# Kernel tuning notes

Hardware: AMD Instinct MI355X
Metric: run time of the kernel (lower is better)

The kernel has to match this reference:

```python
import jax, jax.numpy as jnp
import numpy as np

N_PTS, N_NODES, N_CMP = 2048, 8192, 1024
CHUNK = 4  # cmp columns per scan step; bounds the [P, CHUNK, N] intermediate


def setup_inputs() -> dict:
    key = jax.random.key(0)
    k1, k2 = jax.random.split(key)
    x = jax.random.normal(k1, (N_PTS, N_NODES), dtype=jnp.float32)
    # learned edge states; EDG_NULL == 0, so mask = (states != 0)
    learned_edge_states = jax.random.randint(k2, (N_NODES, N_CMP), 0, 2, dtype=jnp.int32)
    return {"x": x, "learned_edge_states": learned_edge_states}


def _masked_colmax(x, mask):
    """x: [P, N] float; mask: [N, C] bool -> [P, C] max of x over masked nodes per column.

    Columns with no nonzero entries yield 0.0 (original leaves the zero-initialized output).
    Chunked over C to avoid materializing the full [P, N, C] tensor.
    """
    neg_inf = jnp.float32(-jnp.inf)
    P = x.shape[0]
    C = mask.shape[1]
    mask_chunks = mask.T.reshape(C // CHUNK, CHUNK, -1)  # [S, CHUNK, N]

    def step(carry, m):
        # m: [CHUNK, N]; masked max over node axis -> [P, CHUNK]
        vals = jnp.max(jnp.where(m[None, :, :], x[:, None, :], neg_inf), axis=2)
        return carry, vals

    _, out = jax.lax.scan(step, None, mask_chunks)  # [S, P, CHUNK]
    out = jnp.transpose(out, (1, 0, 2)).reshape(P, C)
    has_any = jnp.any(mask, axis=0)  # [C]
    return jnp.where(has_any[None, :], out, jnp.float32(0.0))


def reference(x, learned_edge_states):
    mask = learned_edge_states != 0
    return _masked_colmax(x, mask)
```

## Files before the change

kernel.cpp:

```cpp
#include <hip/hip_runtime.h>
#include <hip/hip_bf16.h>
#include <math.h>

#define N_PTS   2048
#define N_NODES 8192
#define N_CMP   1024
#define CAP     128
#define K_MIN   32
#define K_MAX   112

#define OFF_BITS 0
#define OFF_TOPV (1u << 20)
#define OFF_TOPI (2u << 20)
#define OFF_LEN  (3u << 20)

__device__ __forceinline__ unsigned int float_to_key(float f) {
    unsigned int b = __float_as_uint(f);
    return (b & 0x80000000u) ? ~b : (b | 0x80000000u);
}
__device__ __forceinline__ float key_to_float(unsigned int k) {
    unsigned int b = (k & 0x80000000u) ? (k ^ 0x80000000u) : ~k;
    return __uint_as_float(b);
}

__global__ __launch_bounds__(256) void pack_kernel(const int* __restrict__ states,
                                                   unsigned int* __restrict__ bitsT) {
    int t    = threadIdx.x;
    int lane = t & 63;
    int W    = blockIdx.x * 4 + (t >> 6);
    int n    = W >> 4;
    int cg   = W & 15;
    int s    = states[(size_t)n * N_CMP + cg * 64 + lane];
    unsigned long long m = __ballot(s != 0);
    if (lane == 0) {
        bitsT[n * 32 + cg * 2]     = (unsigned int)(m & 0xffffffffull);
        bitsT[n * 32 + cg * 2 + 1] = (unsigned int)(m >> 32);
    }
}

__global__ __launch_bounds__(256) void select_kernel(const float* __restrict__ x,
                                                     float* __restrict__ topval,
                                                     int* __restrict__ topidx,
                                                     int* __restrict__ toplen) {
    int p = blockIdx.x;
    int t = threadIdx.x;
    const float4* row4 = reinterpret_cast<const float4*>(x + (size_t)p * N_NODES);

    unsigned int key[32];
#pragma unroll
    for (int j = 0; j < 8; j++) {
        float4 v = row4[j * 256 + t];
        key[j * 4 + 0] = float_to_key(v.x);
        key[j * 4 + 1] = float_to_key(v.y);
        key[j * 4 + 2] = float_to_key(v.z);
        key[j * 4 + 3] = float_to_key(v.w);
    }

    __shared__ unsigned int s_cnt[2][4];
    __shared__ unsigned int s_red[4];
    __shared__ unsigned int s_key[CAP];
    __shared__ int          s_id[CAP];
    __shared__ int          s_num;

    unsigned int m = 0;
#pragma unroll
    for (int i = 0; i < 32; i++) m = max(m, key[i]);
#pragma unroll
    for (int d = 1; d < 64; d <<= 1)
        m = max(m, (unsigned int)__shfl_xor((int)m, d));
    if ((t & 63) == 0) s_red[t >> 6] = m;
    __syncthreads();
    unsigned int M = max(max(s_red[0], s_red[1]), max(s_red[2], s_red[3]));
    __syncthreads();

    unsigned int lo = 0, hi = M;
    for (int it = 0; it < 34; ++it) {
        if (hi - lo <= 1) break;
        unsigned int mid;
        if (it == 0) {
            mid = 0xC0200000u;
            if (mid >= hi) mid = hi - 1;
            if (mid <= lo) mid = lo + 1;
        } else {
            mid = lo + ((hi - lo) >> 1);
        }
        int myc = 0;
#pragma unroll
        for (int i = 0; i < 32; i++)
            myc += (int)__popcll(__ballot(key[i] >= mid));
        int par = it & 1;
        if ((t & 63) == 0) s_cnt[par][t >> 6] = (unsigned int)myc;
        __syncthreads();
        int c = (int)(s_cnt[par][0] + s_cnt[par][1] + s_cnt[par][2] + s_cnt[par][3]);
        if (c >= K_MIN) {
            lo = mid;
            if (c <= K_MAX) break;
        } else {
            hi = mid;
        }
    }
    unsigned int T = lo;

    if (t == 0) s_num = 0;
    __syncthreads();
#pragma unroll
    for (int i = 0; i < 32; i++) {
        if (key[i] >= T) {
            int pos = atomicAdd(&s_num, 1);
            if (pos < CAP) {
                s_key[pos] = key[i];
                s_id[pos]  = (i >> 2) * 1024 + (t << 2) + (i & 3);
            }
        }
    }
    __syncthreads();
    int L   = s_num;
    int len = (L > CAP) ? -1 : L;

    if (len > 0 && t < L) {
        unsigned int mk = s_key[t];
        int          mi = s_id[t];
        int r = 0;
        for (int j = 0; j < L; ++j) {
            unsigned int kj = s_key[j];
            r += (int)((kj > mk) | ((kj == mk) & (j < t)));
        }
        topval[(size_t)p * CAP + r] = key_to_float(mk);
        topidx[(size_t)p * CAP + r] = mi;
    }
    if (t == 0) toplen[p] = len;
}

__global__ __launch_bounds__(256) void probe_kernel(const float* __restrict__ x,
                                                    const unsigned int* __restrict__ bitsT,
                                                    const float* __restrict__ topval,
                                                    const int* __restrict__ topidx,
                                                    const int* __restrict__ toplen,
                                                    float* __restrict__ out) {
    int t    = threadIdx.x;
    int lane = t & 63;
    int wid  = t >> 6;
    int b    = blockIdx.x;
    int p    = b >> 2;
    int q    = b & 3;
    int cg   = q * 4 + wid;
    int c    = cg * 64 + lane;
    int w5   = c >> 5;
    int bit  = c & 31;

    __shared__ float s_v[CAP];
    __shared__ int   s_n[CAP];
    __shared__ int   s_len;

    if (t == 0) s_len = toplen[p];
    if (t < CAP) {
        s_v[t] = topval[(size_t)p * CAP + t];
        s_n[t] = topidx[(size_t)p * CAP + t];
    }
    __syncthreads();
    int len = s_len;

    float res  = 0.0f;
    bool  done = false;

    if (len >= 0) {
#pragma unroll 1
        for (int k0 = 0; k0 < len; k0 += 8) {
            int kmax = len - k0;
            if (kmax > 8) kmax = 8;
            unsigned int wb[8];
#pragma unroll
            for (int j = 0; j < 8; j++)
                if (j < kmax) wb[j] = bitsT[s_n[k0 + j] * 32 + w5];
#pragma unroll
            for (int j = 0; j < 8; j++) {
                if (j < kmax) {
                    bool hit = (wb[j] >> bit) & 1u;
                    if (!done && hit) { res = s_v[k0 + j]; done = true; }
                }
            }
            if (__all((int)done)) break;
        }
    }

    if (!done) {
        const float* row = x + (size_t)p * N_NODES;
        float mm = -INFINITY;
        for (int n = 0; n < N_NODES; n++) {
            unsigned int w = bitsT[n * 32 + w5];
            if ((w >> bit) & 1u) mm = fmaxf(mm, row[n]);
        }
        res = (mm == -INFINITY) ? 0.0f : mm;
    }

    out[(size_t)p * N_CMP + c] = res;
}

extern "C" void kernel_launch(void* const* d_in, const int* in_sizes, int n_in,
                              void* d_out, int out_size, void* d_ws, size_t ws_size,
                              hipStream_t stream) {
    const float* x      = (const float*)d_in[0];
    const int*   states = (const int*)d_in[1];
    float*       out    = (float*)d_out;

    unsigned int* bitsT  = (unsigned int*)((char*)d_ws + OFF_BITS);
    float*        topval = (float*)((char*)d_ws + OFF_TOPV);
    int*          topidx = (int*)((char*)d_ws + OFF_TOPI);
    int*          toplen = (int*)((char*)d_ws + OFF_LEN);

    pack_kernel<<<(N_NODES * (N_CMP / 64)) / 4, 256, 0, stream>>>(states, bitsT);
    select_kernel<<<N_PTS, 256, 0, stream>>>(x, topval, topidx, toplen);
    probe_kernel<<<N_PTS * 4, 256, 0, stream>>>(x, bitsT, topval, topidx, toplen, out);
}
```

Before: 146.1 us.

## Fuse pack and select kernels, vectorize pack, one probe block per point

Merges the bit-packing and top-k selection into one launch: the first N_PTS blocks do selection and the rest pack the state matrix. Packing now reads int4 per lane with four ballots and writes two uint4 stores, using a permuted bit layout with matching column-to-word mapping in the probe. The probe kernel now uses one block per point that loops over four column groups, so the shared top-k list is loaded once per point instead of four times. This removes one launch and some redundant loads, but serializes the column groups inside each block and reduces the probe grid size.

```diff
diff --git a/kernel.cpp b/kernel.cpp
--- a/kernel.cpp
+++ b/kernel.cpp
@@ -14,6 +14,7 @@
 #define OFF_TOPI (2u << 20)
 #define OFF_LEN  (3u << 20)
 
+
 __device__ __forceinline__ unsigned int float_to_key(float f) {
     unsigned int b = __float_as_uint(f);
     return (b & 0x80000000u) ? ~b : (b | 0x80000000u);
@@ -23,27 +24,43 @@
     return __uint_as_float(b);
 }
 
-__global__ __launch_bounds__(256) void pack_kernel(const int* __restrict__ states,
-                                                   unsigned int* __restrict__ bitsT) {
-    int t    = threadIdx.x;
-    int lane = t & 63;
-    int W    = blockIdx.x * 4 + (t >> 6);
-    int n    = W >> 4;
-    int cg   = W & 15;
-    int s    = states[(size_t)n * N_CMP + cg * 64 + lane];
-    unsigned long long m = __ballot(s != 0);
-    if (lane == 0) {
-        bitsT[n * 32 + cg * 2]     = (unsigned int)(m & 0xffffffffull);
-        bitsT[n * 32 + cg * 2 + 1] = (unsigned int)(m >> 32);
-    }
-}
-
-__global__ __launch_bounds__(256) void select_kernel(const float* __restrict__ x,
-                                                     float* __restrict__ topval,
-                                                     int* __restrict__ topidx,
-                                                     int* __restrict__ toplen) {
-    int p = blockIdx.x;
+__device__ __forceinline__ int col_word_off(int c) {
+    return (c >> 8) * 8 + (c & 3) * 2 + (((c >> 2) & 63) >> 5);
+}
+__device__ __forceinline__ int col_bit(int c) {
+    return (c >> 2) & 31;
+}
+
+__global__ __launch_bounds__(256) void prep_kernel(const float* __restrict__ x,
+                                                   const int4* __restrict__ states4,
+                                                   unsigned int* __restrict__ bitsT,
+                                                   float* __restrict__ topval,
+                                                   int* __restrict__ topidx,
+                                                   int* __restrict__ toplen) {
+    int b = blockIdx.x;
     int t = threadIdx.x;
+
+    if (b >= N_PTS) {
+        int lane = t & 63;
+        int W = (b - N_PTS) * 4 + (t >> 6);
+        int n = W >> 2;
+        int g = W & 3;
+        int4 v = states4[(size_t)n * 256 + g * 64 + lane];
+        unsigned long long b0 = __ballot(v.x != 0);
+        unsigned long long b1 = __ballot(v.y != 0);
+        unsigned long long b2 = __ballot(v.z != 0);
+        unsigned long long b3 = __ballot(v.w != 0);
+        if (lane == 0) {
+            uint4* dst = reinterpret_cast<uint4*>(bitsT + n * 32 + g * 8);
+            dst[0] = make_uint4((unsigned)b0, (unsigned)(b0 >> 32),
+                                (unsigned)b1, (unsigned)(b1 >> 32));
+            dst[1] = make_uint4((unsigned)b2, (unsigned)(b2 >> 32),
+                                (unsigned)b3, (unsigned)(b3 >> 32));
+        }
+        return;
+    }
+
+    int p = b;
     const float4* row4 = reinterpret_cast<const float4*>(x + (size_t)p * N_NODES);
 
     unsigned int key[32];
@@ -137,16 +154,10 @@
                                                     const int* __restrict__ topidx,
                                                     const int* __restrict__ toplen,
                                                     float* __restrict__ out) {
+    int p    = blockIdx.x;
     int t    = threadIdx.x;
     int lane = t & 63;
-    int wid  = t >> 6;
-    int b    = blockIdx.x;
-    int p    = b >> 2;
-    int q    = b & 3;
-    int cg   = q * 4 + wid;
-    int c    = cg * 64 + lane;
-    int w5   = c >> 5;
-    int bit  = c & 31;
+    int w    = t >> 6;
 
     __shared__ float s_v[CAP];
     __shared__ int   s_n[CAP];
@@ -160,55 +171,63 @@
     __syncthreads();
     int len = s_len;
 
-    float res  = 0.0f;
-    bool  done = false;
-
-    if (len >= 0) {
 #pragma unroll 1
-        for (int k0 = 0; k0 < len; k0 += 8) {
-            int kmax = len - k0;
-            if (kmax > 8) kmax = 8;
-            unsigned int wb[8];
-#pragma unroll
-            for (int j = 0; j < 8; j++)
-                if (j < kmax) wb[j] = bitsT[s_n[k0 + j] * 32 + w5];
-#pragma unroll
-            for (int j = 0; j < 8; j++) {
-                if (j < kmax) {
-                    bool hit = (wb[j] >> bit) & 1u;
-                    if (!done && hit) { res = s_v[k0 + j]; done = true; }
+    for (int i = 0; i < 4; ++i) {
+        int cg   = i * 4 + w;
+        int c    = cg * 64 + lane;
+        int woff = col_word_off(c);
+        int bit  = col_bit(c);
+
+        float res  = 0.0f;
+        bool  done = false;
+
+        if (len >= 0) {
+#pragma unroll 1
+            for (int k0 = 0; k0 < len; k0 += 8) {
+                int kmax = len - k0;
+                if (kmax > 8) kmax = 8;
+                unsigned int wb[8];
+#pragma unroll
+                for (int j = 0; j < 8; j++)
+                    if (j < kmax) wb[j] = bitsT[s_n[k0 + j] * 32 + woff];
+#pragma unroll
+                for (int j = 0; j < 8; j++) {
+                    if (j < kmax) {
+                        bool hit = (wb[j] >> bit) & 1u;
+                        if (!done && hit) { res = s_v[k0 + j]; done = true; }
+                    }
                 }
+                if (__all((int)done)) break;
             }
-            if (__all((int)done)) break;
-        }
-    }
-
-    if (!done) {
-        const float* row = x + (size_t)p * N_NODES;
-        float mm = -INFINITY;
-        for (int n = 0; n < N_NODES; n++) {
-            unsigned int w = bitsT[n * 32 + w5];
-            if ((w >> bit) & 1u) mm = fmaxf(mm, row[n]);
-        }
-        res = (mm == -INFINITY) ? 0.0f : mm;
-    }
-
-    out[(size_t)p * N_CMP + c] = res;
+        }
+
+        if (!done) {
+            const float* row = x + (size_t)p * N_NODES;
+            float mm = -INFINITY;
+            for (int n = 0; n < N_NODES; n++) {
+                unsigned int wd = bitsT[n * 32 + woff];
+                if ((wd >> bit) & 1u) mm = fmaxf(mm, row[n]);
+            }
+            res = (mm == -INFINITY) ? 0.0f : mm;
+        }
+
+        out[(size_t)p * N_CMP + c] = res;
+    }
 }
 
 extern "C" void kernel_launch(void* const* d_in, const int* in_sizes, int n_in,
                               void* d_out, int out_size, void* d_ws, size_t ws_size,
                               hipStream_t stream) {
-    const float* x      = (const float*)d_in[0];
-    const int*   states = (const int*)d_in[1];
-    float*       out    = (float*)d_out;
+    const float* x       = (const float*)d_in[0];
+    const int4*  states4 = (const int4*)d_in[1];
+    float*       out     = (float*)d_out;
 
     unsigned int* bitsT  = (unsigned int*)((char*)d_ws + OFF_BITS);
     float*        topval = (float*)((char*)d_ws + OFF_TOPV);
     int*          topidx = (int*)((char*)d_ws + OFF_TOPI);
     int*          toplen = (int*)((char*)d_ws + OFF_LEN);
 
-    pack_kernel<<<(N_NODES * (N_CMP / 64)) / 4, 256, 0, stream>>>(states, bitsT);
-    select_kernel<<<N_PTS, 256, 0, stream>>>(x, topval, topidx, toplen);
-    probe_kernel<<<N_PTS * 4, 256, 0, stream>>>(x, bitsT, topval, topidx, toplen, out);
-}
+    prep_kernel<<<N_PTS + N_NODES, 256, 0, stream>>>(x, states4, bitsT,
+                                                     topval, topidx, toplen);
+    probe_kernel<<<N_PTS, 256, 0, stream>>>(x, bitsT, topval, topidx, toplen, out);
+}
```

Result: faster. 132.5 us (-9.3%).

## Fuse pack, select and probe into one kernel reading states directly

Applied to the files above, without the earlier changes.

Merges the three kernels into one per-point kernel. The sorted top candidates stay in shared memory and are probed straight against the int32 states matrix rather than a packed bit matrix, so the pack kernel and the workspace round-trips go away. Each block now handles all 1024 columns in four passes. In exchange, every probe reads a full 4-byte state per column (32x more bytes than the bitmask) and gets fewer concurrent blocks. The rare fallback scan now walks the much larger int matrix.

```diff
diff --git a/kernel.cpp b/kernel.cpp
--- a/kernel.cpp
+++ b/kernel.cpp
@@ -9,10 +9,6 @@
 #define K_MIN   32
 #define K_MAX   112
 
-#define OFF_BITS 0
-#define OFF_TOPV (1u << 20)
-#define OFF_TOPI (2u << 20)
-#define OFF_LEN  (3u << 20)
 
 __device__ __forceinline__ unsigned int float_to_key(float f) {
     unsigned int b = __float_as_uint(f);
@@ -23,27 +19,14 @@
     return __uint_as_float(b);
 }
 
-__global__ __launch_bounds__(256) void pack_kernel(const int* __restrict__ states,
-                                                   unsigned int* __restrict__ bitsT) {
+__global__ __launch_bounds__(256) void fused_kernel(const float* __restrict__ x,
+                                                    const int* __restrict__ states,
+                                                    float* __restrict__ out) {
+    int p    = blockIdx.x;
     int t    = threadIdx.x;
     int lane = t & 63;
-    int W    = blockIdx.x * 4 + (t >> 6);
-    int n    = W >> 4;
-    int cg   = W & 15;
-    int s    = states[(size_t)n * N_CMP + cg * 64 + lane];
-    unsigned long long m = __ballot(s != 0);
-    if (lane == 0) {
-        bitsT[n * 32 + cg * 2]     = (unsigned int)(m & 0xffffffffull);
-        bitsT[n * 32 + cg * 2 + 1] = (unsigned int)(m >> 32);
-    }
-}
+    int w    = t >> 6;
 
-__global__ __launch_bounds__(256) void select_kernel(const float* __restrict__ x,
-                                                     float* __restrict__ topval,
-                                                     int* __restrict__ topidx,
-                                                     int* __restrict__ toplen) {
-    int p = blockIdx.x;
-    int t = threadIdx.x;
     const float4* row4 = reinterpret_cast<const float4*>(x + (size_t)p * N_NODES);
 
     unsigned int key[32];
@@ -60,6 +43,8 @@
     __shared__ unsigned int s_red[4];
     __shared__ unsigned int s_key[CAP];
     __shared__ int          s_id[CAP];
+    __shared__ float        s_sv[CAP];
+    __shared__ int          s_sn[CAP];
     __shared__ int          s_num;
 
     unsigned int m = 0;
@@ -68,7 +53,7 @@
 #pragma unroll
     for (int d = 1; d < 64; d <<= 1)
         m = max(m, (unsigned int)__shfl_xor((int)m, d));
-    if ((t & 63) == 0) s_red[t >> 6] = m;
+    if (lane == 0) s_red[w] = m;
     __syncthreads();
     unsigned int M = max(max(s_red[0], s_red[1]), max(s_red[2], s_red[3]));
     __syncthreads();
@@ -89,7 +74,7 @@
         for (int i = 0; i < 32; i++)
             myc += (int)__popcll(__ballot(key[i] >= mid));
         int par = it & 1;
-        if ((t & 63) == 0) s_cnt[par][t >> 6] = (unsigned int)myc;
+        if (lane == 0) s_cnt[par][w] = (unsigned int)myc;
         __syncthreads();
         int c = (int)(s_cnt[par][0] + s_cnt[par][1] + s_cnt[par][2] + s_cnt[par][3]);
         if (c >= K_MIN) {
@@ -125,75 +110,55 @@
             unsigned int kj = s_key[j];
             r += (int)((kj > mk) | ((kj == mk) & (j < t)));
         }
-        topval[(size_t)p * CAP + r] = key_to_float(mk);
-        topidx[(size_t)p * CAP + r] = mi;
-    }
-    if (t == 0) toplen[p] = len;
-}
-
-__global__ __launch_bounds__(256) void probe_kernel(const float* __restrict__ x,
-                                                    const unsigned int* __restrict__ bitsT,
-                                                    const float* __restrict__ topval,
-                                                    const int* __restrict__ topidx,
-                                                    const int* __restrict__ toplen,
-                                                    float* __restrict__ out) {
-    int t    = threadIdx.x;
-    int lane = t & 63;
-    int wid  = t >> 6;
-    int b    = blockIdx.x;
-    int p    = b >> 2;
-    int q    = b & 3;
-    int cg   = q * 4 + wid;
-    int c    = cg * 64 + lane;
-    int w5   = c >> 5;
-    int bit  = c & 31;
-
-    __shared__ float s_v[CAP];
-    __shared__ int   s_n[CAP];
-    __shared__ int   s_len;
-
-    if (t == 0) s_len = toplen[p];
-    if (t < CAP) {
-        s_v[t] = topval[(size_t)p * CAP + t];
-        s_n[t] = topidx[(size_t)p * CAP + t];
+        s_sv[r] = key_to_float(mk);
+        s_sn[r] = mi;
     }
     __syncthreads();
-    int len = s_len;
 
-    float res  = 0.0f;
-    bool  done = false;
+    const int* srow_base = states;
+#pragma unroll 1
+    for (int i = 0; i < 4; ++i) {
+        int cg = i * 4 + w;
+        int c  = cg * 64 + lane;
 
-    if (len >= 0) {
+        float res  = 0.0f;
+        bool  done = false;
+
+        if (len >= 0) {
 #pragma unroll 1
-        for (int k0 = 0; k0 < len; k0 += 8) {
-            int kmax = len - k0;
-            if (kmax > 8) kmax = 8;
-            unsigned int wb[8];
+            for (int k0 = 0; k0 < len; k0 += 8) {
+                int kmax = len - k0;
+                if (kmax > 8) kmax = 8;
+                int sv[8];
 #pragma unroll
-            for (int j = 0; j < 8; j++)
-                if (j < kmax) wb[j] = bitsT[s_n[k0 + j] * 32 + w5];
+                for (int j = 0; j < 8; j++) {
+                    if (j < kmax) {
+                        int n = __builtin_amdgcn_readfirstlane(s_sn[k0 + j]);
+                        sv[j] = srow_base[(size_t)n * N_CMP + c];
+                    }
+                }
 #pragma unroll
-            for (int j = 0; j < 8; j++) {
-                if (j < kmax) {
-                    bool hit = (wb[j] >> bit) & 1u;
-                    if (!done && hit) { res = s_v[k0 + j]; done = true; }
+                for (int j = 0; j < 8; j++) {
+                    if (j < kmax) {
+                        bool hit = (sv[j] != 0);
+                        if (!done && hit) { res = s_sv[k0 + j]; done = true; }
+                    }
                 }
+                if (__all((int)done)) break;
             }
-            if (__all((int)done)) break;
         }
+
+        if (!done) {
+            const float* row = x + (size_t)p * N_NODES;
+            float mm = -INFINITY;
+            for (int n = 0; n < N_NODES; n++) {
+                if (srow_base[(size_t)n * N_CMP + c] != 0) mm = fmaxf(mm, row[n]);
+            }
+            res = (mm == -INFINITY) ? 0.0f : mm;
+        }
+
+        out[(size_t)p * N_CMP + c] = res;
     }
-
-    if (!done) {
-        const float* row = x + (size_t)p * N_NODES;
-        float mm = -INFINITY;
-        for (int n = 0; n < N_NODES; n++) {
-            unsigned int w = bitsT[n * 32 + w5];
-            if ((w >> bit) & 1u) mm = fmaxf(mm, row[n]);
-        }
-        res = (mm == -INFINITY) ? 0.0f : mm;
-    }
-
-    out[(size_t)p * N_CMP + c] = res;
 }
 
 extern "C" void kernel_launch(void* const* d_in, const int* in_sizes, int n_in,
@@ -203,12 +168,5 @@
     const int*   states = (const int*)d_in[1];
     float*       out    = (float*)d_out;
 
-    unsigned int* bitsT  = (unsigned int*)((char*)d_ws + OFF_BITS);
-    float*        topval = (float*)((char*)d_ws + OFF_TOPV);
-    int*          topidx = (int*)((char*)d_ws + OFF_TOPI);
-    int*          toplen = (int*)((char*)d_ws + OFF_LEN);
-
-    pack_kernel<<<(N_NODES * (N_CMP / 64)) / 4, 256, 0, stream>>>(states, bitsT);
-    select_kernel<<<N_PTS, 256, 0, stream>>>(x, topval, topidx, toplen);
-    probe_kernel<<<N_PTS * 4, 256, 0, stream>>>(x, bitsT, topval, topidx, toplen, out);
+    fused_kernel<<<N_PTS, 256, 0, stream>>>(x, states, out);
 }
```

Result: faster. 130.5 us (-10.7%).
